# Performance work log

Measured on AMD Instinct MI355X. Metric: run time of the kernel, lower is better.

## Reference

```python
import jax, jax.numpy as jnp
import numpy as np

B, S, D, NH = 128, 1500, 128, 4
HD = D // NH          # 32
V = 4096
K = 4                 # causal conv kernel size
FF = 192              # round_up(1.3 * 128, 64) per xLSTM FeedForwardConfig
EPS = 1e-5
NEG = -1e30           # acts as -inf for the stabilizer state


def layer_norm(x, w):
    mu = jnp.mean(x, axis=-1, keepdims=True)
    var = jnp.mean((x - mu) ** 2, axis=-1, keepdims=True)
    return (x - mu) * jax.lax.rsqrt(var + EPS) * w


def _forward(seq, emb, conv_w, conv_b, Wi, Wf, Wz, Wo, Ri, Rf, Rz, Ro,
             bi, bf, bz, bo, gn_w, ln1_w, ln2_w, ffn_up, ffn_down, ln_post_w):
    x = emb[seq]                                   # (B,S,D) embedding (row 0 = pad)
    h = layer_norm(x, ln1_w)                       # pre-norm of sLSTM block
    # causal depthwise conv + SiLU feeds the i/f gate projections
    xc = jax.lax.conv_general_dilated(
        h, conv_w, window_strides=(1,), padding=[(K - 1, 0)],
        dimension_numbers=("NWC", "WIO", "NWC"), feature_group_count=D) + conv_b
    xc = jax.nn.silu(xc)

    def headproj(v, W):                            # block-diagonal per-head linear
        return jnp.einsum("bshd,hed->bshe", v.reshape(B, S, NH, HD), W)

    gi, gf = headproj(xc, Wi), headproj(xc, Wf)
    gz, go = headproj(h, Wz), headproj(h, Wo)
    gates = jnp.stack([gi, gf, gz, go], 0).transpose(2, 0, 1, 3, 4)  # (S,4,B,NH,HD)

    def step(carry, g):
        y, c, n, m = carry                         # each (B,NH,HD)
        ir = g[0] + jnp.einsum("bhd,hde->bhe", y, Ri) + bi
        fr = g[1] + jnp.einsum("bhd,hde->bhe", y, Rf) + bf
        zr = g[2] + jnp.einsum("bhd,hde->bhe", y, Rz) + bz
        orr = g[3] + jnp.einsum("bhd,hde->bhe", y, Ro) + bo
        logf = m + jax.nn.log_sigmoid(fr)          # stabilized exponential gating
        m_new = jnp.maximum(ir, logf)
        ig = jnp.exp(ir - m_new)
        fg = jnp.exp(logf - m_new)
        c_new = fg * c + ig * jnp.tanh(zr)
        n_new = fg * n + ig
        y_new = jax.nn.sigmoid(orr) * c_new / n_new
        return (y_new, c_new, n_new, m_new), y_new

    z0 = jnp.zeros((B, NH, HD), jnp.float32)
    m0 = jnp.full((B, NH, HD), NEG, jnp.float32)
    _, ys = jax.lax.scan(step, (z0, z0, z0, m0), gates)  # (S,B,NH,HD)

    y = ys.transpose(1, 0, 2, 3)                   # (B,S,NH,HD)
    mu = jnp.mean(y, axis=-1, keepdims=True)       # multi-head group norm
    var = jnp.mean((y - mu) ** 2, axis=-1, keepdims=True)
    y = (y - mu) * jax.lax.rsqrt(var + EPS) * gn_w.reshape(NH, HD)
    x = x + y.reshape(B, S, D)                     # residual

    h2 = layer_norm(x, ln2_w)                      # gated FFN (GEGLU-style, bias-free)
    u = h2 @ ffn_up                                # (B,S,2*FF)
    x = x + (jax.nn.gelu(u[..., :FF], approximate=False) * u[..., FF:]) @ ffn_down
    x = layer_norm(x, ln_post_w)                   # post-blocks LayerNorm
    return jnp.mean(x, axis=1)                     # mean pool -> (B,D)


def setup_inputs():
    key = jax.random.key(0)
    ks = jax.random.split(key, 24)
    sc = lambda k, shp, s=0.05: jax.random.normal(k, shp, jnp.float32) * s
    emb = sc(ks[0], (V, D), 0.1).at[0].set(0.0)    # padding_idx=0
    return {
        "seq": jax.random.randint(ks[1], (B, S), 0, V),
        "emb": emb,
        "conv_w": sc(ks[2], (K, 1, D), 0.1),
        "conv_b": sc(ks[3], (D,), 0.02),
        "Wi": sc(ks[4], (NH, HD, HD), 0.1),
        "Wf": sc(ks[5], (NH, HD, HD), 0.1),
        "Wz": sc(ks[6], (NH, HD, HD), 0.1),
        "Wo": sc(ks[7], (NH, HD, HD), 0.1),
        "Ri": sc(ks[8], (NH, HD, HD), 0.1),
        "Rf": sc(ks[9], (NH, HD, HD), 0.1),
        "Rz": sc(ks[10], (NH, HD, HD), 0.1),
        "Ro": sc(ks[11], (NH, HD, HD), 0.1),
        "bi": sc(ks[12], (NH, HD), 0.02),
        "bf": jnp.tile(jnp.linspace(3.0, 6.0, HD, dtype=jnp.float32), (NH, 1)),
        "bz": sc(ks[14], (NH, HD), 0.02),
        "bo": sc(ks[15], (NH, HD), 0.02),
        "gn_w": jnp.ones((D,), jnp.float32),
        "ln1_w": jnp.ones((D,), jnp.float32),
        "ln2_w": jnp.ones((D,), jnp.float32),
        "ffn_up": sc(ks[16], (D, 2 * FF), 0.08),
        "ffn_down": sc(ks[17], (FF, D), 0.08),
        "ln_post_w": jnp.ones((D,), jnp.float32),
    }


def reference(seq, emb, conv_w, conv_b, Wi, Wf, Wz, Wo, Ri, Rf, Rz, Ro,
              bi, bf, bz, bo, gn_w, ln1_w, ln2_w, ffn_up, ffn_down, ln_post_w):
    return _forward(seq, emb, conv_w, conv_b, Wi, Wf, Wz, Wo, Ri, Rf, Rz, Ro,
                    bi, bf, bz, bo, gn_w, ln1_w, ln2_w, ffn_up, ffn_down, ln_post_w)
```

## Files before the change

### kernel.cpp

```cpp
#include <hip/hip_runtime.h>
#include <hip/hip_bf16.h>
#include <math.h>

#define BB   128
#define SS   1500
#define DD   128
#define NHH  4
#define HDD  32
#define FFF  192
#define EPSV 1e-5f
#define GXCH 16

typedef __bf16   bf16x8 __attribute__((ext_vector_type(8)));
typedef float    f32x4  __attribute__((ext_vector_type(4)));
typedef float    f32x2  __attribute__((ext_vector_type(2)));
typedef _Float16 f16x2  __attribute__((ext_vector_type(2)));

__global__ void __launch_bounds__(256) k_stats(
    const int* __restrict__ seq, const float* __restrict__ emb,
    float* __restrict__ stats)
{
    const int w = threadIdx.x >> 6, l = threadIdx.x & 63;
    for (int t = blockIdx.x * 4 + w; t < BB * SS; t += gridDim.x * 4) {
        int tok = seq[t];
        f32x2 v = *(const f32x2*)(emb + (size_t)tok * DD + 2 * l);
        float s1 = v[0] + v[1], s2 = v[0] * v[0] + v[1] * v[1];
        #pragma unroll
        for (int mm = 1; mm <= 32; mm <<= 1) {
            s1 += __shfl_xor(s1, mm);
            s2 += __shfl_xor(s2, mm);
        }
        if (l == 0) {
            float mu  = s1 * (1.f / 128.f);
            float var = s2 * (1.f / 128.f) - mu * mu;
            stats[2 * t]     = mu;
            stats[2 * t + 1] = rsqrtf(var + EPSV);
        }
    }
}

__global__ void k_prep(const float* __restrict__ up, const float* __restrict__ down,
                       __bf16* __restrict__ wupT, __bf16* __restrict__ wdnT)
{
    int i = blockIdx.x * 256 + threadIdx.x;
    if (i < 384 * 128) {
        int n = i >> 7, k = i & 127;
        wupT[i] = (__bf16)up[k * 384 + n];
    }
    int j = i - 384 * 128;
    if (j >= 0 && j < 128 * 192) {
        int n = j / 192, k = j - n * 192;
        wdnT[j] = (__bf16)down[k * 128 + n];
    }
}

__global__ void __launch_bounds__(256, 2) k_gx(
    const int* __restrict__ seq, const float* __restrict__ emb,
    const float* __restrict__ stats,
    const float* __restrict__ convw, const float* __restrict__ convb,
    const float* __restrict__ ln1w,
    const float* __restrict__ Wi, const float* __restrict__ Wf,
    const float* __restrict__ Wz, const float* __restrict__ Wo,
    const float* __restrict__ bi, const float* __restrict__ bfv,
    const float* __restrict__ bz, const float* __restrict__ bo,
    unsigned int* __restrict__ gx)
{
    __shared__ float hl[(GXCH + 3) * 128];

    const int tid = threadIdx.x;
    const int w   = tid >> 6;
    const int l   = tid & 63;
    const int p   = l >> 5;
    const int e   = l & 31;
    const int b   = blockIdx.y;
    const int s0  = blockIdx.x * GXCH;
    const int ch  = w * 32 + e;

    const float* W0 = p ? Wf : Wi;
    const float* W1 = p ? Wo : Wz;
    float wr0[32], wr1[32];
    #pragma unroll
    for (int q = 0; q < 32; ++q) {
        wr0[q] = W0[w * 1024 + e * 32 + q];
        wr1[q] = W1[w * 1024 + e * 32 + q];
    }
    const float b0 = (p ? bfv : bi)[w * 32 + e];
    const float b1 = (p ? bo  : bz)[w * 32 + e];
    const float cb = convb[ch];
    float cw[4];
    #pragma unroll
    for (int k = 0; k < 4; ++k) cw[k] = convw[k * DD + ch];

    for (int idx = tid; idx < (GXCH + 3) * 128; idx += 256) {
        int r = idx >> 7, d = idx & 127;
        int sg = s0 - 3 + r;
        float hv = 0.f;
        if (sg >= 0 && sg < SS) {
            int tok = seq[b * SS + sg];
            float mu = stats[2 * (b * SS + sg)];
            float rs = stats[2 * (b * SS + sg) + 1];
            hv = (emb[(size_t)tok * DD + d] - mu) * rs * ln1w[d];
        }
        hl[idx] = hv;
    }
    __syncthreads();

    for (int t = 0; t < GXCH; ++t) {
        if (s0 + t >= SS) break;
        float xc = cb;
        #pragma unroll
        for (int k = 0; k < 4; ++k) xc = fmaf(hl[(t + k) * 128 + ch], cw[k], xc);
        xc = xc / (1.f + __expf(-xc));
        float hv = hl[(t + 3) * 128 + ch];

        float a0 = b0, a1 = b1;
        #pragma unroll
        for (int q = 0; q < 32; ++q) {
            float x0 = __builtin_bit_cast(float,
                         __builtin_amdgcn_readlane(__builtin_bit_cast(int, xc), q));
            float x1 = __builtin_bit_cast(float,
                         __builtin_amdgcn_readlane(__builtin_bit_cast(int, hv), q));
            a0 = fmaf(x0, wr0[q], a0);
            a1 = fmaf(x1, wr1[q], a1);
        }
        float a0p = __shfl_xor(a0, 32);
        float a1p = __shfl_xor(a1, 32);
        if (l < 32) {
            f16x2 w0; w0[0] = (_Float16)a0; w0[1] = (_Float16)a0p;
            f16x2 w1; w1[0] = (_Float16)a1; w1[1] = (_Float16)a1p;
            size_t base = ((size_t)(b * 4 + w) * SS + s0 + t) * 64;
            gx[base + l]      = __builtin_bit_cast(unsigned int, w0);
            gx[base + 32 + l] = __builtin_bit_cast(unsigned int, w1);
        }
    }
}

__global__ void __launch_bounds__(64, 1) k_scan2(
    const unsigned int* __restrict__ gx,
    const float* __restrict__ Ri, const float* __restrict__ Rf,
    const float* __restrict__ Rz, const float* __restrict__ Ro,
    _Float16* __restrict__ yout)
{
    const int l  = threadIdx.x;
    const int up = l >> 5;
    const int e  = l & 31;
    const int bh = blockIdx.x;
    const int b  = bh >> 2, h = bh & 3;

    const float* RA = up ? Rz : Ri;
    const float* RB = up ? Ro : Rf;
    float ra[32], rb[32];
    #pragma unroll
    for (int q = 0; q < 32; ++q) {
        ra[q] = RA[h * 1024 + q * 32 + e];
        rb[q] = RB[h * 1024 + q * 32 + e];
    }

    float y = 0.f, c = 0.f, n = 0.f, m = -1e30f;

    const unsigned int* gp = gx + (size_t)bh * SS * 64 + l;
    _Float16* yp = yout + (size_t)b * SS * DD + h * 32 + e;

    unsigned int pf[4];
    #pragma unroll
    for (int u = 0; u < 4; ++u) pf[u] = gp[(size_t)u * 64];

    for (int s0 = 0; s0 < SS; s0 += 4) {
        #pragma unroll
        for (int u = 0; u < 4; ++u) {
            int s = s0 + u;
            unsigned int gword = pf[u];
            int spf = (s + 4 < SS) ? s + 4 : SS - 1;
            pf[u] = gp[(size_t)spf * 64];

            f16x2 gh = __builtin_bit_cast(f16x2, gword);

            float yq[32];
            #pragma unroll
            for (int q = 0; q < 32; ++q)
                yq[q] = __builtin_bit_cast(float,
                          __builtin_amdgcn_readlane(__builtin_bit_cast(int, y), q));

            float a0 = (float)gh[0], a1 = 0.f, a2 = 0.f, a3 = 0.f;
            float c0 = (float)gh[1], c1 = 0.f, c2 = 0.f, c3 = 0.f;
            #pragma unroll
            for (int q = 0; q < 8; ++q) {
                a0 = fmaf(yq[q],      ra[q],      a0);
                a1 = fmaf(yq[q + 8],  ra[q + 8],  a1);
                a2 = fmaf(yq[q + 16], ra[q + 16], a2);
                a3 = fmaf(yq[q + 24], ra[q + 24], a3);
                c0 = fmaf(yq[q],      rb[q],      c0);
                c1 = fmaf(yq[q + 8],  rb[q + 8],  c1);
                c2 = fmaf(yq[q + 16], rb[q + 16], c2);
                c3 = fmaf(yq[q + 24], rb[q + 24], c3);
            }
            float accA = (a0 + a1) + (a2 + a3);
            float accB = (c0 + c1) + (c2 + c3);

            float zr  = __shfl_xor(accA, 32);
            float orr = __shfl_xor(accB, 32);
            float ir  = accA, fr = accB;

            float lsig = fminf(fr, 0.f) - __logf(1.f + __expf(-fabsf(fr)));
            float lf   = m + lsig;
            float mn   = fmaxf(ir, lf);
            float ig   = __expf(ir - mn);
            float fg   = __expf(lf - mn);
            float e2   = __expf(2.f * zr);
            float zt   = 1.f - 2.f / (e2 + 1.f);
            c = fg * c + ig * zt;
            n = fg * n + ig;
            float so = 1.f / (1.f + __expf(-orr));
            y = so * c / n;
            m = mn;

            if (!up) yp[(size_t)s * DD] = (_Float16)y;
        }
    }
}

__global__ void __launch_bounds__(64) k_scan_fused(
    const int* __restrict__ seq, const float* __restrict__ emb,
    const float* __restrict__ stats,
    const float* __restrict__ convw, const float* __restrict__ convb,
    const float* __restrict__ ln1w,
    const float* __restrict__ Wi, const float* __restrict__ Wf,
    const float* __restrict__ Wz, const float* __restrict__ Wo,
    const float* __restrict__ Ri, const float* __restrict__ Rf,
    const float* __restrict__ Rz, const float* __restrict__ Ro,
    const float* __restrict__ bi, const float* __restrict__ bfv,
    const float* __restrict__ bz, const float* __restrict__ bo,
    _Float16* __restrict__ yout)
{
    __shared__ int   stok[SS];
    __shared__ float smu[SS];
    __shared__ float srs[SS];

    const int lane = threadIdx.x;
    const int half = lane >> 5;
    const int e    = lane & 31;
    const int d0   = half * 16;
    const int bh   = blockIdx.x;
    const int b    = bh >> 2, h = bh & 3;
    const int ch   = h * 32 + e;

    for (int i = lane; i < SS; i += 64) {
        stok[i] = seq[b * SS + i];
        f32x2 st = *(const f32x2*)(stats + (size_t)(b * SS + i) * 2);
        smu[i] = st[0];
        srs[i] = st[1];
    }
    __syncthreads();

    float wi[16], wf[16], wz[16], wo[16];
    float ri[16], rf[16], rz[16], ro[16];
    {
        const float* Wib = Wi + h * 1024 + e * 32 + d0;
        const float* Wfb = Wf + h * 1024 + e * 32 + d0;
        const float* Wzb = Wz + h * 1024 + e * 32 + d0;
        const float* Wob = Wo + h * 1024 + e * 32 + d0;
        const float* Rib = Ri + h * 1024 + d0 * 32 + e;
        const float* Rfb = Rf + h * 1024 + d0 * 32 + e;
        const float* Rzb = Rz + h * 1024 + d0 * 32 + e;
        const float* Rob = Ro + h * 1024 + d0 * 32 + e;
        #pragma unroll
        for (int q = 0; q < 16; ++q) {
            wi[q] = Wib[q]; wf[q] = Wfb[q]; wz[q] = Wzb[q]; wo[q] = Wob[q];
            ri[q] = Rib[q * 32]; rf[q] = Rfb[q * 32];
            rz[q] = Rzb[q * 32]; ro[q] = Rob[q * 32];
        }
    }
    const float biv = bi [h * 32 + e];
    const float bfb = bfv[h * 32 + e];
    const float bzv = bz [h * 32 + e];
    const float bov = bo [h * 32 + e];
    const float lnv = ln1w[ch];
    const float cbr = convb[ch];
    const float cw0 = convw[0 * DD + ch], cw1 = convw[1 * DD + ch];
    const float cw2 = convw[2 * DD + ch], cw3 = convw[3 * DD + ch];

    float y = 0.f, c = 0.f, n = 0.f, m = -1e30f;
    float hm1 = 0.f, hm2 = 0.f, hm3 = 0.f;

    _Float16* yp = yout + ((size_t)b * SS) * DD + ch;

    float x0 = emb[(size_t)stok[0] * DD + ch];
    float x1 = (SS > 1) ? emb[(size_t)stok[1] * DD + ch] : 0.f;

    for (int s = 0; s < SS; ++s) {
        float x2 = 0.f;
        if (s + 2 < SS) x2 = emb[(size_t)stok[s + 2] * DD + ch];

        float h0 = (x0 - smu[s]) * srs[s] * lnv;
        float xc = cbr;
        xc = fmaf(hm3, cw0, xc);
        xc = fmaf(hm2, cw1, xc);
        xc = fmaf(hm1, cw2, xc);
        xc = fmaf(h0,  cw3, xc);
        xc = xc / (1.f + __expf(-xc));
        hm3 = hm2; hm2 = hm1; hm1 = h0;

        float ir = 0.f, fr = 0.f, zr = 0.f, orr = 0.f;
        #pragma unroll
        for (int q = 0; q < 16; ++q) {
            float xd = __shfl(xc, d0 + q, 32);
            float hd = __shfl(h0, d0 + q, 32);
            float yd = __shfl(y,  d0 + q, 32);
            ir  = fmaf(xd, wi[q], ir);
            fr  = fmaf(xd, wf[q], fr);
            zr  = fmaf(hd, wz[q], zr);
            orr = fmaf(hd, wo[q], orr);
            ir  = fmaf(yd, ri[q], ir);
            fr  = fmaf(yd, rf[q], fr);
            rz[q] = rz[q];
            zr  = fmaf(yd, rz[q], zr);
            orr = fmaf(yd, ro[q], orr);
        }
        ir  += __shfl_xor(ir, 32);
        fr  += __shfl_xor(fr, 32);
        zr  += __shfl_xor(zr, 32);
        orr += __shfl_xor(orr, 32);
        ir += biv; fr += bfb; zr += bzv; orr += bov;

        float lsig = fminf(fr, 0.f) - __logf(1.f + __expf(-fabsf(fr)));
        float lf   = m + lsig;
        float mn   = fmaxf(ir, lf);
        float ig   = __expf(ir - mn);
        float fg   = __expf(lf - mn);
        float e2   = __expf(2.f * zr);
        float zt   = 1.f - 2.f / (e2 + 1.f);
        c = fg * c + ig * zt;
        n = fg * n + ig;
        float so = 1.f / (1.f + __expf(-orr));
        y = so * c / n;
        m = mn;

        if (half == 0) yp[(size_t)s * DD] = (_Float16)y;
        x0 = x1; x1 = x2;
    }
}

__global__ void __launch_bounds__(256) k_ffn(
    const int* __restrict__ seq, const float* __restrict__ emb,
    const _Float16* __restrict__ yb, const float* __restrict__ gnw,
    const float* __restrict__ ln2w, const float* __restrict__ lnpw,
    const __bf16* __restrict__ wupT, const __bf16* __restrict__ wdnT,
    float* __restrict__ out)
{
    __shared__ __bf16 h2l[32 * 136];
    __shared__ __bf16 fl [32 * 200];
    __shared__ float  xrl[32 * 132];

    const int tid = threadIdx.x;
    const int w   = tid >> 6, l = tid & 63;
    const int lr  = l & 15,  lh = l >> 4;
    const int b   = blockIdx.y;
    const int t0  = blockIdx.x * 32;

    const float gw0 = gnw[2 * l],  gw1 = gnw[2 * l + 1];
    const float l2w0 = ln2w[2 * l], l2w1 = ln2w[2 * l + 1];
    const float lpw0 = lnpw[2 * l], lpw1 = lnpw[2 * l + 1];

    for (int it = 0; it < 8; ++it) {
        int tt = it * 4 + w;
        int stok = t0 + tt;
        float x0 = 0.f, x1 = 0.f, y0 = 0.f, y1 = 0.f;
        if (stok < SS) {
            int tk = seq[b * SS + stok];
            f32x2 xv = *(const f32x2*)(emb + (size_t)tk * DD + 2 * l);
            f16x2 yv = *(const f16x2*)(yb + ((size_t)b * SS + stok) * DD + 2 * l);
            x0 = xv[0]; x1 = xv[1]; y0 = (float)yv[0]; y1 = (float)yv[1];
        }
        float s1 = y0 + y1, s2 = y0 * y0 + y1 * y1;
        #pragma unroll
        for (int mm = 1; mm <= 8; mm <<= 1) { s1 += __shfl_xor(s1, mm); s2 += __shfl_xor(s2, mm); }
        float mu  = s1 * (1.f / 32.f);
        float var = s2 * (1.f / 32.f) - mu * mu;
        float inv = rsqrtf(var + EPSV);
        float xr0 = x0 + (y0 - mu) * inv * gw0;
        float xr1 = x1 + (y1 - mu) * inv * gw1;
        float t1 = xr0 + xr1, t2 = xr0 * xr0 + xr1 * xr1;
        #pragma unroll
        for (int mm = 1; mm <= 32; mm <<= 1) { t1 += __shfl_xor(t1, mm); t2 += __shfl_xor(t2, mm); }
        float mu2  = t1 * (1.f / 128.f);
        float var2 = t2 * (1.f / 128.f) - mu2 * mu2;
        float inv2 = rsqrtf(var2 + EPSV);
        xrl[tt * 132 + 2 * l]     = xr0;
        xrl[tt * 132 + 2 * l + 1] = xr1;
        h2l[tt * 136 + 2 * l]     = (__bf16)((xr0 - mu2) * inv2 * l2w0);
        h2l[tt * 136 + 2 * l + 1] = (__bf16)((xr1 - mu2) * inv2 * l2w1);
    }
    __syncthreads();

    f32x4 acc1[2][6];
    #pragma unroll
    for (int mt = 0; mt < 2; ++mt)
        #pragma unroll
        for (int nt = 0; nt < 6; ++nt)
            acc1[mt][nt] = (f32x4){0.f, 0.f, 0.f, 0.f};

    #pragma unroll
    for (int kk = 0; kk < 4; ++kk) {
        int k0 = kk * 32;
        bf16x8 bfr[6];
        #pragma unroll
        for (int nt = 0; nt < 6; ++nt) {
            int colbase = (nt < 3) ? (w * 48 + nt * 16) : (192 + w * 48 + (nt - 3) * 16);
            bfr[nt] = *(const bf16x8*)(wupT + (colbase + lr) * DD + k0 + lh * 8);
        }
        #pragma unroll
        for (int mt = 0; mt < 2; ++mt) {
            bf16x8 afr = *(const bf16x8*)(h2l + (mt * 16 + lr) * 136 + k0 + lh * 8);
            #pragma unroll
            for (int nt = 0; nt < 6; ++nt)
                acc1[mt][nt] = __builtin_amdgcn_mfma_f32_16x16x32_bf16(afr, bfr[nt], acc1[mt][nt], 0, 0, 0);
        }
    }

    #pragma unroll
    for (int mt = 0; mt < 2; ++mt)
        #pragma unroll
        for (int nt = 0; nt < 3; ++nt)
            #pragma unroll
            for (int j = 0; j < 4; ++j) {
                int r = mt * 16 + lh * 4 + j;
                int cN = w * 48 + nt * 16 + lr;
                float a  = acc1[mt][nt][j];
                float bv = acc1[mt][nt + 3][j];
                float ge = 0.5f * a * (1.f + erff(a * 0.70710678118f));
                fl[r * 200 + cN] = (__bf16)(ge * bv);
            }
    __syncthreads();

    f32x4 acc2[2][2];
    #pragma unroll
    for (int mt = 0; mt < 2; ++mt) {
        acc2[mt][0] = (f32x4){0.f, 0.f, 0.f, 0.f};
        acc2[mt][1] = (f32x4){0.f, 0.f, 0.f, 0.f};
    }
    #pragma unroll
    for (int kk = 0; kk < 6; ++kk) {
        int k0 = kk * 32;
        bf16x8 bfr2[2];
        #pragma unroll
        for (int nt = 0; nt < 2; ++nt)
            bfr2[nt] = *(const bf16x8*)(wdnT + (w * 32 + nt * 16 + lr) * FFF + k0 + lh * 8);
        #pragma unroll
        for (int mt = 0; mt < 2; ++mt) {
            bf16x8 afr = *(const bf16x8*)(fl + (mt * 16 + lr) * 200 + k0 + lh * 8);
            #pragma unroll
            for (int nt = 0; nt < 2; ++nt)
                acc2[mt][nt] = __builtin_amdgcn_mfma_f32_16x16x32_bf16(afr, bfr2[nt], acc2[mt][nt], 0, 0, 0);
        }
    }
    #pragma unroll
    for (int mt = 0; mt < 2; ++mt)
        #pragma unroll
        for (int nt = 0; nt < 2; ++nt)
            #pragma unroll
            for (int j = 0; j < 4; ++j) {
                int r  = mt * 16 + lh * 4 + j;
                int cN = w * 32 + nt * 16 + lr;
                xrl[r * 132 + cN] += acc2[mt][nt][j];
            }
    __syncthreads();

    float p0 = 0.f, p1 = 0.f;
    for (int it = 0; it < 8; ++it) {
        int tt = it * 4 + w;
        int stok = t0 + tt;
        if (stok >= SS) continue;
        float xr0 = xrl[tt * 132 + 2 * l];
        float xr1 = xrl[tt * 132 + 2 * l + 1];
        float t1 = xr0 + xr1, t2 = xr0 * xr0 + xr1 * xr1;
        #pragma unroll
        for (int mm = 1; mm <= 32; mm <<= 1) { t1 += __shfl_xor(t1, mm); t2 += __shfl_xor(t2, mm); }
        float mu  = t1 * (1.f / 128.f);
        float var = t2 * (1.f / 128.f) - mu * mu;
        float inv = rsqrtf(var + EPSV);
        p0 += (xr0 - mu) * inv * lpw0;
        p1 += (xr1 - mu) * inv * lpw1;
    }
    atomicAdd(out + b * DD + 2 * l,     p0 * (1.f / SS));
    atomicAdd(out + b * DD + 2 * l + 1, p1 * (1.f / SS));
}

extern "C" void kernel_launch(void* const* d_in, const int* in_sizes, int n_in,
                              void* d_out, int out_size, void* d_ws, size_t ws_size,
                              hipStream_t stream)
{
    const int*   seq   = (const int*)  d_in[0];
    const float* emb   = (const float*)d_in[1];
    const float* convw = (const float*)d_in[2];
    const float* convb = (const float*)d_in[3];
    const float* Wi    = (const float*)d_in[4];
    const float* Wf    = (const float*)d_in[5];
    const float* Wz    = (const float*)d_in[6];
    const float* Wo    = (const float*)d_in[7];
    const float* Ri    = (const float*)d_in[8];
    const float* Rf    = (const float*)d_in[9];
    const float* Rz    = (const float*)d_in[10];
    const float* Ro    = (const float*)d_in[11];
    const float* bi    = (const float*)d_in[12];
    const float* bfp   = (const float*)d_in[13];
    const float* bz    = (const float*)d_in[14];
    const float* bo    = (const float*)d_in[15];
    const float* gnw   = (const float*)d_in[16];
    const float* ln1w  = (const float*)d_in[17];
    const float* ln2w  = (const float*)d_in[18];
    const float* ffup  = (const float*)d_in[19];
    const float* ffdn  = (const float*)d_in[20];
    const float* lnpw  = (const float*)d_in[21];
    float* out = (float*)d_out;

    char* ws = (char*)d_ws;
    float*        stats = (float*)ws;
    _Float16*     yws   = (_Float16*)(ws + 1536000);
    __bf16*       wupT  = (__bf16*)(ws + 50688000);
    __bf16*       wdnT  = (__bf16*)(ws + 50786304);
    unsigned int* gxb   = (unsigned int*)(ws + 50835456);
    const size_t NEED_GX = 50835456ull + 196608000ull;

    hipMemsetAsync(d_out, 0, (size_t)BB * DD * sizeof(float), stream);

    hipLaunchKernelGGL(k_stats, dim3(2048), dim3(256), 0, stream, seq, emb, stats);
    hipLaunchKernelGGL(k_prep, dim3(288), dim3(256), 0, stream, ffup, ffdn, wupT, wdnT);

    if (ws_size >= NEED_GX) {
        hipLaunchKernelGGL(k_gx, dim3((SS + GXCH - 1) / GXCH, BB), dim3(256), 0, stream,
                           seq, emb, stats, convw, convb, ln1w,
                           Wi, Wf, Wz, Wo, bi, bfp, bz, bo, gxb);
        hipLaunchKernelGGL(k_scan2, dim3(512), dim3(64), 0, stream,
                           gxb, Ri, Rf, Rz, Ro, yws);
    } else {
        hipLaunchKernelGGL(k_scan_fused, dim3(512), dim3(64), 0, stream,
                           seq, emb, stats, convw, convb, ln1w,
                           Wi, Wf, Wz, Wo, Ri, Rf, Rz, Ro, bi, bfp, bz, bo, yws);
    }
    hipLaunchKernelGGL(k_ffn, dim3(47, 128), dim3(256), 0, stream,
                       seq, emb, yws, gnw, ln2w, lnpw, wupT, wdnT, out);
}
```

Baseline: 1.137 ms.

## Broadcast gate inputs via LDS vector reads and use fast reciprocals

In the gate-projection kernel, per-lane readlane broadcasts of the conv/SiLU output and normed input are replaced with vectorized LDS reads from a small shared buffer, and the dot products are split into two accumulators each. The weight arrays in the gx and scan kernels are pinned to VGPRs with empty asm constraints so they are not rematerialized or spilled. IEEE divisions in SiLU, tanh, sigmoid and y=c/n are replaced with hardware approximate reciprocals, which cuts latency on the serial scan path at some cost in precision. A leftover no-op self-assignment in the fused scan kernel is also removed.

```diff
diff --git a/kernel.cpp b/kernel.cpp
--- a/kernel.cpp
+++ b/kernel.cpp
@@ -66,6 +66,7 @@
     unsigned int* __restrict__ gx)
 {
     __shared__ float hl[(GXCH + 3) * 128];
+    __shared__ float xcl[4 * 32];
 
     const int tid = threadIdx.x;
     const int w   = tid >> 6;
@@ -83,6 +84,11 @@
     for (int q = 0; q < 32; ++q) {
         wr0[q] = W0[w * 1024 + e * 32 + q];
         wr1[q] = W1[w * 1024 + e * 32 + q];
+    }
+    #pragma unroll
+    for (int q = 0; q < 32; ++q) {
+        asm volatile("" : "+v"(wr0[q]));
+        asm volatile("" : "+v"(wr1[q]));
     }
     const float b0 = (p ? bfv : bi)[w * 32 + e];
     const float b1 = (p ? bo  : bz)[w * 32 + e];
@@ -110,24 +116,33 @@
         float xc = cb;
         #pragma unroll
         for (int k = 0; k < 4; ++k) xc = fmaf(hl[(t + k) * 128 + ch], cw[k], xc);
-        xc = xc / (1.f + __expf(-xc));
-        float hv = hl[(t + 3) * 128 + ch];
-
-        float a0 = b0, a1 = b1;
-        #pragma unroll
-        for (int q = 0; q < 32; ++q) {
-            float x0 = __builtin_bit_cast(float,
-                         __builtin_amdgcn_readlane(__builtin_bit_cast(int, xc), q));
-            float x1 = __builtin_bit_cast(float,
-                         __builtin_amdgcn_readlane(__builtin_bit_cast(int, hv), q));
-            a0 = fmaf(x0, wr0[q], a0);
-            a1 = fmaf(x1, wr1[q], a1);
-        }
-        float a0p = __shfl_xor(a0, 32);
-        float a1p = __shfl_xor(a1, 32);
+        xc = xc * __builtin_amdgcn_rcpf(1.f + __expf(-xc));
+        if (l < 32) xcl[w * 32 + e] = xc;
+
+        const f32x4* xs = (const f32x4*)(xcl + w * 32);
+        const f32x4* hs = (const f32x4*)(hl + (t + 3) * 128 + w * 32);
+
+        float a0 = b0, a1 = 0.f, c0 = b1, c1 = 0.f;
+        #pragma unroll
+        for (int q8 = 0; q8 < 8; q8 += 2) {
+            f32x4 xv0 = xs[q8], xv1 = xs[q8 + 1];
+            f32x4 hv0 = hs[q8], hv1 = hs[q8 + 1];
+            #pragma unroll
+            for (int j = 0; j < 4; ++j) {
+                a0 = fmaf(xv0[j], wr0[4 * q8 + j],     a0);
+                a1 = fmaf(xv1[j], wr0[4 * q8 + 4 + j], a1);
+                c0 = fmaf(hv0[j], wr1[4 * q8 + j],     c0);
+                c1 = fmaf(hv1[j], wr1[4 * q8 + 4 + j], c1);
+            }
+        }
+        float a = a0 + a1;
+        float cz = c0 + c1;
+
+        float ap = __shfl_xor(a, 32);
+        float cp = __shfl_xor(cz, 32);
         if (l < 32) {
-            f16x2 w0; w0[0] = (_Float16)a0; w0[1] = (_Float16)a0p;
-            f16x2 w1; w1[0] = (_Float16)a1; w1[1] = (_Float16)a1p;
+            f16x2 w0; w0[0] = (_Float16)a;  w0[1] = (_Float16)ap;
+            f16x2 w1; w1[0] = (_Float16)cz; w1[1] = (_Float16)cp;
             size_t base = ((size_t)(b * 4 + w) * SS + s0 + t) * 64;
             gx[base + l]      = __builtin_bit_cast(unsigned int, w0);
             gx[base + 32 + l] = __builtin_bit_cast(unsigned int, w1);
@@ -154,6 +169,11 @@
     for (int q = 0; q < 32; ++q) {
         ra[q] = RA[h * 1024 + q * 32 + e];
         rb[q] = RB[h * 1024 + q * 32 + e];
+    }
+    #pragma unroll
+    for (int q = 0; q < 32; ++q) {
+        asm volatile("" : "+v"(ra[q]));
+        asm volatile("" : "+v"(rb[q]));
     }
 
     float y = 0.f, c = 0.f, n = 0.f, m = -1e30f;
@@ -207,11 +227,11 @@
             float ig   = __expf(ir - mn);
             float fg   = __expf(lf - mn);
             float e2   = __expf(2.f * zr);
-            float zt   = 1.f - 2.f / (e2 + 1.f);
+            float zt   = 1.f - 2.f * __builtin_amdgcn_rcpf(e2 + 1.f);
             c = fg * c + ig * zt;
             n = fg * n + ig;
-            float so = 1.f / (1.f + __expf(-orr));
-            y = so * c / n;
+            float so = __builtin_amdgcn_rcpf(1.f + __expf(-orr));
+            y = so * c * __builtin_amdgcn_rcpf(n);
             m = mn;
 
             if (!up) yp[(size_t)s * DD] = (_Float16)y;
@@ -312,7 +332,6 @@
             orr = fmaf(hd, wo[q], orr);
             ir  = fmaf(yd, ri[q], ir);
             fr  = fmaf(yd, rf[q], fr);
-            rz[q] = rz[q];
             zr  = fmaf(yd, rz[q], zr);
             orr = fmaf(yd, ro[q], orr);
         }
```

New measurement: 1.041 ms. -8.5%, faster.
